# Optimization experiments

Measured on AMD Instinct MI355X. Metric: run time of the kernel, lower is better.

Reference implementation:

```python
import jax, jax.numpy as jnp
import numpy as np


def _moe(x, router_w, bias, shared_up, shared_down, expert_up, expert_down, topk):
    B, T, C = x.shape
    xf = x.reshape(-1, C)                      # (N, C)
    N = xf.shape[0]
    E = router_w.shape[1]
    P = N * topk
    capacity = 2 * P // E

    # --- shared SwiGLU expert (always active); torch Expert order: (y, gate) = chunk ---
    y, g = jnp.split(xf @ shared_up, 2, axis=-1)
    shared = (jax.nn.silu(g) * y) @ shared_down          # (N, C)

    # --- sigmoid top-k gate with (detached) load-balance bias ---
    scores = jax.nn.sigmoid(xf @ router_w)               # (N, E)
    _, topk_idx = jax.lax.top_k(jax.lax.stop_gradient(scores) + bias, topk)  # (N, K)
    w = jnp.take_along_axis(scores, topk_idx, axis=-1)
    w = w / jnp.sum(w, axis=-1, keepdims=True)           # route_scale = 1.0

    # --- token permutation: sort (token, k) pairs by expert id (stable) ---
    pair_e = topk_idx.reshape(-1)                        # (P,)
    pair_t = jnp.repeat(jnp.arange(N), topk)             # (P,) original token ids
    pair_w = w.reshape(-1)
    order = jnp.argsort(pair_e, stable=True)
    se, st, sw = pair_e[order], pair_t[order], pair_w[order]
    counts = jnp.bincount(pair_e, length=E)              # tokens per expert
    offs = jnp.cumsum(counts) - counts                   # start of each expert's slice
    pos = jnp.arange(P) - offs[se]                       # slot within expert group (< capacity)

    # --- grouped-GEMM expert execution via capacity-padded (E, cap, C) buffer ---
    xbuf = jnp.zeros((E, capacity, C), x.dtype).at[se, pos].set(xf[st])
    up = jnp.einsum('epc,ech->eph', xbuf, expert_up)     # (E, cap, 2*He)
    y2, g2 = jnp.split(up, 2, axis=-1)
    h = jax.nn.silu(g2) * y2
    oe = jnp.einsum('eph,ehc->epc', h, expert_down)      # (E, cap, C)

    # --- weighted combine back to original token positions ---
    out_pairs = oe[se, pos] * sw[:, None]                # (P, C)
    out = jnp.zeros_like(xf).at[st].add(out_pairs)
    return (shared + out).reshape(B, T, C)


def setup_inputs() -> dict:
    key = jax.random.key(0)
    ks = jax.random.split(key, 6)
    B, T, C, E, He, Hs, K = 2, 2048, 1024, 64, 512, 1024, 8
    s = 0.02
    return {
        'x': jax.random.normal(ks[0], (B, T, C), jnp.float32),
        'router_w': jax.random.normal(ks[1], (C, E), jnp.float32) * s,
        'bias': jnp.zeros((E,), jnp.float32),
        'shared_up': jax.random.normal(ks[2], (C, 2 * Hs), jnp.float32) * s,
        'shared_down': jax.random.normal(ks[3], (Hs, C), jnp.float32) * s,
        'expert_up': jax.random.normal(ks[4], (E, C, 2 * He), jnp.float32) * s,
        'expert_down': jax.random.normal(ks[5], (E, He, C), jnp.float32) * s,
        'topk': K,
    }


def reference(x, router_w, bias, shared_up, shared_down, expert_up, expert_down, topk):
    return _moe(x, router_w, bias, shared_up, shared_down, expert_up, expert_down, topk)
```

## Files before the change

kernel.cpp:

```cpp
#include <hip/hip_runtime.h>
#include <stdint.h>

#define N_TOK 4096
#define C_DIM 1024
#define E_NUM 64
#define TOPK  8
#define P_PAIR (N_TOK*TOPK)
#define RMAX  40960

typedef __attribute__((ext_vector_type(8))) short bf16x8;
typedef __attribute__((ext_vector_type(4))) float f32x4;

__device__ __forceinline__ uint32_t f2bf(float f){
  uint32_t u = __builtin_bit_cast(uint32_t, f);
  u += 0x7fffu + ((u >> 16) & 1u);
  return u >> 16;
}
__device__ __forceinline__ uint32_t pack2bf(float a, float b){
  uint32_t ua = __builtin_bit_cast(uint32_t, a);
  uint32_t ub = __builtin_bit_cast(uint32_t, b);
  ua += 0x7fffu + ((ua >> 16) & 1u);
  ub += 0x7fffu + ((ub >> 16) & 1u);
  return (ua >> 16) | (ub & 0xffff0000u);
}
__device__ __forceinline__ float bf2f(uint32_t u){
  return __builtin_bit_cast(float, u << 16);
}

__global__ __launch_bounds__(256) void router_scores(
    const float* __restrict__ x, const float* __restrict__ rw, double* __restrict__ scores)
{
  __shared__ float xs[16][C_DIM];
  int t0 = blockIdx.x * 16;
  for (int r = 0; r < 16; ++r) {
    int c = threadIdx.x * 4;
    *(float4*)&xs[r][c] = *(const float4*)&x[(size_t)(t0 + r)*C_DIM + c];
  }
  __syncthreads();
  int e = threadIdx.x & 63;
  int slot = threadIdx.x >> 6;
  double acc0=0, acc1=0, acc2=0, acc3=0;
  for (int c = 0; c < C_DIM; ++c) {
    double w = (double)rw[c*E_NUM + e];
    acc0 += (double)xs[slot    ][c] * w;
    acc1 += (double)xs[slot + 4][c] * w;
    acc2 += (double)xs[slot + 8][c] * w;
    acc3 += (double)xs[slot +12][c] * w;
  }
  scores[(size_t)(t0 + slot     )*E_NUM + e] = 1.0/(1.0 + exp(-acc0));
  scores[(size_t)(t0 + slot +  4)*E_NUM + e] = 1.0/(1.0 + exp(-acc1));
  scores[(size_t)(t0 + slot +  8)*E_NUM + e] = 1.0/(1.0 + exp(-acc2));
  scores[(size_t)(t0 + slot + 12)*E_NUM + e] = 1.0/(1.0 + exp(-acc3));
}

__global__ __launch_bounds__(256) void router_topk(
    const double* __restrict__ scores, const float* __restrict__ bias,
    int* __restrict__ topk_idx, float* __restrict__ topk_w, int* __restrict__ counts)
{
  int t = blockIdx.x * blockDim.x + threadIdx.x;
  if (t >= N_TOK) return;
  const double* s = scores + (size_t)t*E_NUM;
  unsigned long long chosen = 0;
  int idx[TOPK]; double val[TOPK]; double wsum = 0;
  for (int k = 0; k < TOPK; ++k) {
    double best = -1e300; int bi = 0;
    for (int e = 0; e < E_NUM; ++e) {
      if ((chosen >> e) & 1ull) continue;
      double v = s[e] + (double)bias[e];
      if (v > best) { best = v; bi = e; }
    }
    chosen |= 1ull << bi;
    idx[k] = bi;
    val[k] = s[bi];
    wsum += s[bi];
    atomicAdd(&counts[bi], 1);
  }
  for (int k = 0; k < TOPK; ++k) {
    topk_idx[t*TOPK + k] = idx[k];
    topk_w[t*TOPK + k] = (float)(val[k] / wsum);
  }
}

__global__ __launch_bounds__(64) void scan_offsets(const int* __restrict__ counts, int* __restrict__ pad_off)
{
  if (threadIdx.x == 0) {
    int acc = 0;
    for (int e = 0; e < E_NUM; ++e) { pad_off[e] = acc; acc += (counts[e] + 127) & ~127; }
    pad_off[E_NUM] = acc;
  }
}

__global__ __launch_bounds__(256) void build_rows(
    const int* __restrict__ topk_idx, const float* __restrict__ topk_w,
    const int* __restrict__ counts, const int* __restrict__ pad_off,
    int* __restrict__ row_token, float* __restrict__ row_wt, int* __restrict__ row_pair)
{
  int e = blockIdx.x;
  int base = pad_off[e];
  __shared__ int wsum_l[4];
  __shared__ int run_s;
  if (threadIdx.x == 0) run_s = 0;
  int lane = threadIdx.x & 63, wv = threadIdx.x >> 6;
  for (int p0 = 0; p0 < P_PAIR; p0 += 256) {
    int p = p0 + threadIdx.x;
    bool flag = (topk_idx[p] == e);
    unsigned long long mb = __ballot(flag);
    int rank = __popcll(mb & ((1ull << lane) - 1ull));
    if (lane == 0) wsum_l[wv] = __popcll(mb);
    __syncthreads();
    int wbase = 0;
    #pragma unroll
    for (int i = 0; i < 4; ++i) if (i < wv) wbase += wsum_l[i];
    int tot = wsum_l[0] + wsum_l[1] + wsum_l[2] + wsum_l[3];
    int run = run_s;
    if (flag) {
      int row = base + run + wbase + rank;
      row_token[row] = p >> 3;
      row_wt[row]    = topk_w[p];
      row_pair[row]  = p;
    }
    __syncthreads();
    if (threadIdx.x == 0) run_s = run + tot;
  }
  __syncthreads();
  int cnt = counts[e];
  int pc = pad_off[e+1] - base;
  for (int r = cnt + threadIdx.x; r < pc; r += 256) {
    row_token[base + r] = -1;
    row_wt[base + r] = 0.f;
    row_pair[base + r] = -1;
  }
}

template<bool SHARED>
__global__ __launch_bounds__(256) void up_gemm(
    const float* __restrict__ X, const float* __restrict__ Wb,
    const int* __restrict__ row_token, const int* __restrict__ pad_off,
    uint16_t* __restrict__ hout, int ldB, int gOff, int ldh)
{
  __shared__ __align__(16) short As[128*32];
  __shared__ __align__(16) short Bs[128*32];
  __shared__ int tok_lds[128];

  const int tid = threadIdx.x;
  const int e = blockIdx.z;
  int row0;
  if constexpr (SHARED) {
    row0 = blockIdx.y * 128;
  } else {
    int pbase = pad_off[e];
    int pcnt  = pad_off[e+1] - pbase;
    if ((int)blockIdx.y * 128 >= pcnt) return;
    row0 = pbase + blockIdx.y * 128;
  }
  const float* W = Wb + (size_t)e * C_DIM * ldB;
  const int c0 = blockIdx.x * 64;

  if (tid < 128) {
    if constexpr (SHARED) tok_lds[tid] = row0 + tid;
    else                  tok_lds[tid] = row_token[row0 + tid];
  }

  const int lane = tid & 63, wid = tid >> 6;
  const int wm = (wid >> 1) * 64, wn = (wid & 1) * 64;
  const int q = lane >> 4, l15 = lane & 15;

  f32x4 acc[4][4];
  #pragma unroll
  for (int i = 0; i < 4; ++i)
    #pragma unroll
    for (int j = 0; j < 4; ++j) { f32x4 z = {0.f,0.f,0.f,0.f}; acc[i][j] = z; }

  const int lnB = tid & 127;
  const int ucB = ((lnB & 16) ? gOff : 0) + c0 + ((lnB >> 5) << 4) + (lnB & 15);
  const int kgB0 = tid >> 7;
  const int sA = tid & 7, rbA = tid >> 3;

  for (int kt = 0; kt < C_DIM/32; ++kt) {
    const int k0 = kt * 32;
    __syncthreads();
    #pragma unroll
    for (int p = 0; p < 4; ++p) {
      int r = p*32 + rbA;
      int tok = tok_lds[r];
      float4 v = {0.f,0.f,0.f,0.f};
      if (SHARED || tok >= 0) v = *(const float4*)&X[(size_t)tok*C_DIM + k0 + sA*4];
      uint32_t lo = pack2bf(v.x, v.y), hi = pack2bf(v.z, v.w);
      int off = r*32 + ((((sA>>1) ^ (r&3))) << 3) + (sA&1)*4;
      *(uint2*)&As[off] = make_uint2(lo, hi);
    }
    #pragma unroll
    for (int p = 0; p < 4; ++p) {
      int kg = kgB0 + 2*p;
      int kk = k0 + kg*4;
      float v0 = W[(size_t)(kk+0)*ldB + ucB];
      float v1 = W[(size_t)(kk+1)*ldB + ucB];
      float v2 = W[(size_t)(kk+2)*ldB + ucB];
      float v3 = W[(size_t)(kk+3)*ldB + ucB];
      uint32_t lo = pack2bf(v0, v1), hi = pack2bf(v2, v3);
      int off = lnB*32 + ((((kg>>1) ^ (lnB&3))) << 3) + (kg&1)*4;
      *(uint2*)&Bs[off] = make_uint2(lo, hi);
    }
    __syncthreads();
    bf16x8 a[4], b[4];
    #pragma unroll
    for (int mi = 0; mi < 4; ++mi) {
      int r = wm + mi*16 + l15;
      a[mi] = *(const bf16x8*)&As[r*32 + ((q ^ (r&3)) << 3)];
    }
    #pragma unroll
    for (int ni = 0; ni < 4; ++ni) {
      int r = wn + ni*16 + l15;
      b[ni] = *(const bf16x8*)&Bs[r*32 + ((q ^ (r&3)) << 3)];
    }
    #pragma unroll
    for (int mi = 0; mi < 4; ++mi)
      #pragma unroll
      for (int ni = 0; ni < 4; ++ni)
        acc[mi][ni] = __builtin_amdgcn_mfma_f32_16x16x32_bf16(a[mi], b[ni], acc[mi][ni], 0, 0, 0);
  }

  #pragma unroll
  for (int mi = 0; mi < 4; ++mi) {
    int rowb = row0 + wm + mi*16 + q*4;
    #pragma unroll
    for (int jj = 0; jj < 2; ++jj) {
      f32x4 yv = acc[mi][2*jj], gv = acc[mi][2*jj+1];
      int j = (wn >> 5) + jj;
      int hc = c0 + j*16 + l15;
      #pragma unroll
      for (int r = 0; r < 4; ++r) {
        float g = gv[r];
        float sg = 1.f / (1.f + __expf(-g));
        float h = yv[r] * (g * sg);
        hout[(size_t)(rowb + r) * ldh + hc] = (uint16_t)f2bf(h);
      }
    }
  }
}

template<bool SHARED>
__global__ __launch_bounds__(256) void down_gemm(
    const uint16_t* __restrict__ H, const float* __restrict__ Wb,
    const float* __restrict__ row_wt, const int* __restrict__ row_pair,
    const int* __restrict__ pad_off, void* __restrict__ outp,
    int ldh, int Kdim)
{
  __shared__ __align__(16) short As[128*32];
  __shared__ __align__(16) short Bs[128*32];
  __shared__ float wt_lds[128];
  __shared__ int pr_lds[128];

  const int tid = threadIdx.x;
  const int e = blockIdx.z;
  int row0;
  if constexpr (SHARED) {
    row0 = blockIdx.y * 128;
  } else {
    int pbase = pad_off[e];
    int pcnt  = pad_off[e+1] - pbase;
    if ((int)blockIdx.y * 128 >= pcnt) return;
    row0 = pbase + blockIdx.y * 128;
  }
  const float* W = Wb + (size_t)e * Kdim * 1024;
  const int c0 = blockIdx.x * 128;

  if (!SHARED && tid < 128) {
    wt_lds[tid] = row_wt[row0 + tid];
    pr_lds[tid] = row_pair[row0 + tid];
  }

  const int lane = tid & 63, wid = tid >> 6;
  const int wm = (wid >> 1) * 64, wn = (wid & 1) * 64;
  const int q = lane >> 4, l15 = lane & 15;

  f32x4 acc[4][4];
  #pragma unroll
  for (int i = 0; i < 4; ++i)
    #pragma unroll
    for (int j = 0; j < 4; ++j) { f32x4 z = {0.f,0.f,0.f,0.f}; acc[i][j] = z; }

  const int lnB = tid & 127;
  const int kgB0 = tid >> 7;
  const int rbA = tid >> 2, cA = tid & 3;

  const int KT = Kdim >> 5;
  for (int kt = 0; kt < KT; ++kt) {
    const int k0 = kt * 32;
    __syncthreads();
    #pragma unroll
    for (int p = 0; p < 2; ++p) {
      int r = p*64 + rbA;
      uint4 v = *(const uint4*)&H[(size_t)(row0 + r)*ldh + k0 + cA*8];
      int off = r*32 + ((cA ^ (r&3)) << 3);
      *(uint4*)&As[off] = v;
    }
    #pragma unroll
    for (int p = 0; p < 4; ++p) {
      int kg = kgB0 + 2*p;
      int kk = k0 + kg*4;
      float v0 = W[(size_t)(kk+0)*1024 + c0 + lnB];
      float v1 = W[(size_t)(kk+1)*1024 + c0 + lnB];
      float v2 = W[(size_t)(kk+2)*1024 + c0 + lnB];
      float v3 = W[(size_t)(kk+3)*1024 + c0 + lnB];
      uint32_t lo = pack2bf(v0, v1), hi = pack2bf(v2, v3);
      int off = lnB*32 + ((((kg>>1) ^ (lnB&3))) << 3) + (kg&1)*4;
      *(uint2*)&Bs[off] = make_uint2(lo, hi);
    }
    __syncthreads();
    bf16x8 a[4], b[4];
    #pragma unroll
    for (int mi = 0; mi < 4; ++mi) {
      int r = wm + mi*16 + l15;
      a[mi] = *(const bf16x8*)&As[r*32 + ((q ^ (r&3)) << 3)];
    }
    #pragma unroll
    for (int ni = 0; ni < 4; ++ni) {
      int r = wn + ni*16 + l15;
      b[ni] = *(const bf16x8*)&Bs[r*32 + ((q ^ (r&3)) << 3)];
    }
    #pragma unroll
    for (int mi = 0; mi < 4; ++mi)
      #pragma unroll
      for (int ni = 0; ni < 4; ++ni)
        acc[mi][ni] = __builtin_amdgcn_mfma_f32_16x16x32_bf16(a[mi], b[ni], acc[mi][ni], 0, 0, 0);
  }

  if constexpr (SHARED) {
    float* out = (float*)outp;
    #pragma unroll
    for (int mi = 0; mi < 4; ++mi) {
      int rowb = row0 + wm + mi*16 + q*4;
      #pragma unroll
      for (int r = 0; r < 4; ++r)
        #pragma unroll
        for (int ni = 0; ni < 4; ++ni)
          out[(size_t)(rowb + r)*1024 + c0 + wn + ni*16 + l15] = acc[mi][ni][r];
    }
  } else {
    uint16_t* ob = (uint16_t*)outp;
    #pragma unroll
    for (int mi = 0; mi < 4; ++mi) {
      int rloc = wm + mi*16 + q*4;
      #pragma unroll
      for (int r = 0; r < 4; ++r) {
        float wt = wt_lds[rloc + r];
        int pr = pr_lds[rloc + r];
        if (pr >= 0) {
          #pragma unroll
          for (int ni = 0; ni < 4; ++ni)
            ob[(size_t)pr*1024 + c0 + wn + ni*16 + l15] = (uint16_t)f2bf(acc[mi][ni][r] * wt);
        }
      }
    }
  }
}

__global__ __launch_bounds__(256) void combine_kernel(
    const uint16_t* __restrict__ obuf, float* __restrict__ out)
{
  int t = blockIdx.x;
  int c = threadIdx.x * 4;
  float a0=0, a1=0, a2=0, a3=0;
  #pragma unroll
  for (int k = 0; k < TOPK; ++k) {
    uint2 v = *(const uint2*)&obuf[((size_t)t*TOPK + k)*1024 + c];
    a0 += bf2f(v.x & 0xffffu); a1 += bf2f(v.x >> 16);
    a2 += bf2f(v.y & 0xffffu); a3 += bf2f(v.y >> 16);
  }
  float4 o = *(float4*)&out[(size_t)t*1024 + c];
  o.x += a0; o.y += a1; o.z += a2; o.w += a3;
  *(float4*)&out[(size_t)t*1024 + c] = o;
}

extern "C" void kernel_launch(void* const* d_in, const int* in_sizes, int n_in,
                              void* d_out, int out_size, void* d_ws, size_t ws_size,
                              hipStream_t stream)
{
  const float* x           = (const float*)d_in[0];
  const float* router_w    = (const float*)d_in[1];
  const float* bias        = (const float*)d_in[2];
  const float* shared_up   = (const float*)d_in[3];
  const float* shared_down = (const float*)d_in[4];
  const float* expert_up   = (const float*)d_in[5];
  const float* expert_down = (const float*)d_in[6];
  float* out = (float*)d_out;

  char* w = (char*)d_ws;
  auto alloc = [&](size_t bytes) -> void* {
    void* p = (void*)w;
    w += (bytes + 255) & ~(size_t)255;
    return p;
  };
  double*  scores    = (double*)  alloc((size_t)N_TOK*E_NUM*8);
  int*     topk_idx  = (int*)     alloc((size_t)N_TOK*TOPK*4);
  float*   topk_w    = (float*)   alloc((size_t)N_TOK*TOPK*4);
  int*     counts    = (int*)     alloc(E_NUM*4);
  int*     pad_off   = (int*)     alloc((E_NUM+1)*4);
  int*     row_token = (int*)     alloc((size_t)RMAX*4);
  float*   row_wt    = (float*)   alloc((size_t)RMAX*4);
  int*     row_pair  = (int*)     alloc((size_t)RMAX*4);
  uint16_t* hbuf     = (uint16_t*)alloc((size_t)RMAX*512*2);
  uint16_t* hsbuf    = (uint16_t*)alloc((size_t)N_TOK*1024*2);
  uint16_t* obuf     = (uint16_t*)alloc((size_t)P_PAIR*1024*2);

  hipMemsetAsync(counts, 0, E_NUM*4, stream);
  router_scores<<<N_TOK/16, 256, 0, stream>>>(x, router_w, scores);
  router_topk<<<N_TOK/256, 256, 0, stream>>>(scores, bias, topk_idx, topk_w, counts);
  scan_offsets<<<1, 64, 0, stream>>>(counts, pad_off);
  build_rows<<<E_NUM, 256, 0, stream>>>(topk_idx, topk_w, counts, pad_off, row_token, row_wt, row_pair);

  up_gemm<false><<<dim3(8, 8, 64), 256, 0, stream>>>(x, expert_up, row_token, pad_off, hbuf, 1024, 512, 512);
  up_gemm<true><<<dim3(16, 32, 1), 256, 0, stream>>>(x, shared_up, nullptr, nullptr, hsbuf, 2048, 1024, 1024);
  down_gemm<true><<<dim3(8, 32, 1), 256, 0, stream>>>(hsbuf, shared_down, nullptr, nullptr, nullptr, (void*)out, 1024, 1024);
  down_gemm<false><<<dim3(8, 8, 64), 256, 0, stream>>>(hbuf, expert_down, row_wt, row_pair, pad_off, (void*)obuf, 512, 512);
  combine_kernel<<<N_TOK, 256, 0, stream>>>(obuf, out);
}
```

Baseline: 1.299 ms.

## Pre-convert weights to transposed bf16 and stream GEMM tiles via global_load_lds

Adds per-call kernels that convert x to bf16 and transpose-convert all expert and shared weights to bf16 in K-contiguous layout. The GEMMs then fill LDS with direct 16-byte global-to-LDS async copies in MFMA fragment order, replacing the per-element fp32 loads and in-register bf16 packing. The expert grids are also flattened with a remapped block order that interleaves experts. The trade-off is an extra pass that reads all fp32 weights (about 400MB) and writes them back as bf16 on every call, in exchange for cheaper, coalesced GEMM operand loads.

Result: faster. 1.117 ms (-14.0%).

```diff
diff --git a/kernel.cpp b/kernel.cpp
--- a/kernel.cpp
+++ b/kernel.cpp
@@ -10,21 +10,27 @@
 
 typedef __attribute__((ext_vector_type(8))) short bf16x8;
 typedef __attribute__((ext_vector_type(4))) float f32x4;
-
-__device__ __forceinline__ uint32_t f2bf(float f){
-  uint32_t u = __builtin_bit_cast(uint32_t, f);
+typedef uint32_t u32;
+
+__device__ __forceinline__ u32 f2bf(float f){
+  u32 u = __builtin_bit_cast(u32, f);
   u += 0x7fffu + ((u >> 16) & 1u);
   return u >> 16;
 }
-__device__ __forceinline__ uint32_t pack2bf(float a, float b){
-  uint32_t ua = __builtin_bit_cast(uint32_t, a);
-  uint32_t ub = __builtin_bit_cast(uint32_t, b);
+__device__ __forceinline__ u32 pack2bf(float a, float b){
+  u32 ua = __builtin_bit_cast(u32, a);
+  u32 ub = __builtin_bit_cast(u32, b);
   ua += 0x7fffu + ((ua >> 16) & 1u);
   ub += 0x7fffu + ((ub >> 16) & 1u);
   return (ua >> 16) | (ub & 0xffff0000u);
 }
-__device__ __forceinline__ float bf2f(uint32_t u){
+__device__ __forceinline__ float bf2f(u32 u){
   return __builtin_bit_cast(float, u << 16);
+}
+
+__device__ __forceinline__ void async_copy16(const void* g, void* l) {
+  __builtin_amdgcn_global_load_lds((const __attribute__((address_space(1))) u32*)g,
+                                   (__attribute__((address_space(3))) u32*)l, 16, 0, 0);
 }
 
 __global__ __launch_bounds__(256) void router_scores(
@@ -132,38 +138,94 @@
   }
 }
 
+__global__ __launch_bounds__(256) void cvt_x(const float* __restrict__ in, uint16_t* __restrict__ out)
+{
+  int i = blockIdx.x * 256 + threadIdx.x;
+  float4 a = *(const float4*)&in[(size_t)i*8];
+  float4 b = *(const float4*)&in[(size_t)i*8 + 4];
+  uint4 o;
+  o.x = pack2bf(a.x, a.y); o.y = pack2bf(a.z, a.w);
+  o.z = pack2bf(b.x, b.y); o.w = pack2bf(b.z, b.w);
+  *(uint4*)&out[(size_t)i*8] = o;
+}
+
+__global__ __launch_bounds__(256) void transpose_cvt(
+    const float* __restrict__ in, uint16_t* __restrict__ out, int R, int Cc)
+{
+  __shared__ uint16_t tile[64][72];
+  const size_t bo = (size_t)blockIdx.z * R * Cc;
+  int c0 = blockIdx.x * 64;
+  int r0 = blockIdx.y * 64;
+  int tx = threadIdx.x & 15, ty = threadIdx.x >> 4;
+  #pragma unroll
+  for (int i = 0; i < 4; ++i) {
+    int r = ty + i*16;
+    float4 v = *(const float4*)&in[bo + (size_t)(r0 + r)*Cc + c0 + tx*4];
+    *(uint2*)&tile[r][tx*4] = make_uint2(pack2bf(v.x, v.y), pack2bf(v.z, v.w));
+  }
+  __syncthreads();
+  #pragma unroll
+  for (int i = 0; i < 2; ++i) {
+    int u = threadIdx.x + 256*i;
+    int c = u >> 3, rc = u & 7;
+    uint16_t tmp[8];
+    #pragma unroll
+    for (int j = 0; j < 8; ++j) tmp[j] = tile[rc*8 + j][c];
+    *(uint4*)&out[bo + (size_t)(c0 + c)*R + r0 + rc*8] = *(uint4*)tmp;
+  }
+}
+
 template<bool SHARED>
-__global__ __launch_bounds__(256) void up_gemm(
-    const float* __restrict__ X, const float* __restrict__ Wb,
+__global__ __launch_bounds__(256) void up_gemm2(
+    const uint16_t* __restrict__ Xb, const uint16_t* __restrict__ Wt,
     const int* __restrict__ row_token, const int* __restrict__ pad_off,
-    uint16_t* __restrict__ hout, int ldB, int gOff, int ldh)
-{
-  __shared__ __align__(16) short As[128*32];
-  __shared__ __align__(16) short Bs[128*32];
+    uint16_t* __restrict__ hout, int He, int ldh)
+{
+  __shared__ __align__(16) uint16_t As[8*512];
+  __shared__ __align__(16) uint16_t Bs[8*512];
   __shared__ int tok_lds[128];
 
   const int tid = threadIdx.x;
-  const int e = blockIdx.z;
+  int e, xt, yt;
+  if constexpr (SHARED) {
+    e = 0; xt = blockIdx.x; yt = blockIdx.y;
+  } else {
+    int f = blockIdx.x;
+    int s = f >> 3;
+    e = (f & 7) * 8 + (s >> 6);
+    int unit = s & 63;
+    xt = unit & 7; yt = unit >> 3;
+  }
   int row0;
   if constexpr (SHARED) {
-    row0 = blockIdx.y * 128;
+    row0 = yt * 128;
   } else {
-    int pbase = pad_off[e];
-    int pcnt  = pad_off[e+1] - pbase;
-    if ((int)blockIdx.y * 128 >= pcnt) return;
-    row0 = pbase + blockIdx.y * 128;
-  }
-  const float* W = Wb + (size_t)e * C_DIM * ldB;
-  const int c0 = blockIdx.x * 64;
-
-  if (tid < 128) {
-    if constexpr (SHARED) tok_lds[tid] = row0 + tid;
-    else                  tok_lds[tid] = row_token[row0 + tid];
-  }
+    int pbase = pad_off[e], pcnt = pad_off[e+1] - pbase;
+    if (yt * 128 >= pcnt) return;
+    row0 = pbase + yt * 128;
+  }
+  const int c0 = xt * 64;
+  const uint16_t* W = Wt + (size_t)e * (2*He) * 1024;
+
+  if (tid < 128)
+    tok_lds[tid] = SHARED ? (row0 + tid) : row_token[row0 + tid];
+  __syncthreads();
 
   const int lane = tid & 63, wid = tid >> 6;
+  const int l15 = lane & 15, q = lane >> 4;
   const int wm = (wid >> 1) * 64, wn = (wid & 1) * 64;
-  const int q = lane >> 4, l15 = lane & 15;
+
+  const int gp0 = 2*wid, gp1 = 2*wid + 1;
+  int tA0 = tok_lds[gp0*16 + l15]; if (tA0 < 0) tA0 = 0;
+  int tA1 = tok_lds[gp1*16 + l15]; if (tA1 < 0) tA1 = 0;
+  const uint16_t* gA0 = Xb + (size_t)tA0*C_DIM + q*8;
+  const uint16_t* gA1 = Xb + (size_t)tA1*C_DIM + q*8;
+  const int nc0 = ((gp0 & 1) ? He : 0) + c0 + (gp0 >> 1)*16 + l15;
+  const int nc1 = ((gp1 & 1) ? He : 0) + c0 + (gp1 >> 1)*16 + l15;
+  const uint16_t* gB0 = W + (size_t)nc0*C_DIM + q*8;
+  const uint16_t* gB1 = W + (size_t)nc1*C_DIM + q*8;
+  uint16_t* lA0 = &As[gp0*512]; uint16_t* lA1 = &As[gp1*512];
+  uint16_t* lB0 = &Bs[gp0*512]; uint16_t* lB1 = &Bs[gp1*512];
 
   f32x4 acc[4][4];
   #pragma unroll
@@ -171,48 +233,20 @@
     #pragma unroll
     for (int j = 0; j < 4; ++j) { f32x4 z = {0.f,0.f,0.f,0.f}; acc[i][j] = z; }
 
-  const int lnB = tid & 127;
-  const int ucB = ((lnB & 16) ? gOff : 0) + c0 + ((lnB >> 5) << 4) + (lnB & 15);
-  const int kgB0 = tid >> 7;
-  const int sA = tid & 7, rbA = tid >> 3;
-
-  for (int kt = 0; kt < C_DIM/32; ++kt) {
-    const int k0 = kt * 32;
-    __syncthreads();
-    #pragma unroll
-    for (int p = 0; p < 4; ++p) {
-      int r = p*32 + rbA;
-      int tok = tok_lds[r];
-      float4 v = {0.f,0.f,0.f,0.f};
-      if (SHARED || tok >= 0) v = *(const float4*)&X[(size_t)tok*C_DIM + k0 + sA*4];
-      uint32_t lo = pack2bf(v.x, v.y), hi = pack2bf(v.z, v.w);
-      int off = r*32 + ((((sA>>1) ^ (r&3))) << 3) + (sA&1)*4;
-      *(uint2*)&As[off] = make_uint2(lo, hi);
-    }
-    #pragma unroll
-    for (int p = 0; p < 4; ++p) {
-      int kg = kgB0 + 2*p;
-      int kk = k0 + kg*4;
-      float v0 = W[(size_t)(kk+0)*ldB + ucB];
-      float v1 = W[(size_t)(kk+1)*ldB + ucB];
-      float v2 = W[(size_t)(kk+2)*ldB + ucB];
-      float v3 = W[(size_t)(kk+3)*ldB + ucB];
-      uint32_t lo = pack2bf(v0, v1), hi = pack2bf(v2, v3);
-      int off = lnB*32 + ((((kg>>1) ^ (lnB&3))) << 3) + (kg&1)*4;
-      *(uint2*)&Bs[off] = make_uint2(lo, hi);
-    }
+  for (int k0 = 0; k0 < C_DIM; k0 += 32) {
+    __syncthreads();
+    async_copy16(gA0 + k0, lA0);
+    async_copy16(gA1 + k0, lA1);
+    async_copy16(gB0 + k0, lB0);
+    async_copy16(gB1 + k0, lB1);
     __syncthreads();
     bf16x8 a[4], b[4];
     #pragma unroll
-    for (int mi = 0; mi < 4; ++mi) {
-      int r = wm + mi*16 + l15;
-      a[mi] = *(const bf16x8*)&As[r*32 + ((q ^ (r&3)) << 3)];
-    }
-    #pragma unroll
-    for (int ni = 0; ni < 4; ++ni) {
-      int r = wn + ni*16 + l15;
-      b[ni] = *(const bf16x8*)&Bs[r*32 + ((q ^ (r&3)) << 3)];
-    }
+    for (int mi = 0; mi < 4; ++mi)
+      a[mi] = *(const bf16x8*)&As[(wm/16 + mi)*512 + lane*8];
+    #pragma unroll
+    for (int ni = 0; ni < 4; ++ni)
+      b[ni] = *(const bf16x8*)&Bs[(wn/16 + ni)*512 + lane*8];
     #pragma unroll
     for (int mi = 0; mi < 4; ++mi)
       #pragma unroll
@@ -240,39 +274,56 @@
 }
 
 template<bool SHARED>
-__global__ __launch_bounds__(256) void down_gemm(
-    const uint16_t* __restrict__ H, const float* __restrict__ Wb,
+__global__ __launch_bounds__(256) void down_gemm2(
+    const uint16_t* __restrict__ H, const uint16_t* __restrict__ Wt,
     const float* __restrict__ row_wt, const int* __restrict__ row_pair,
     const int* __restrict__ pad_off, void* __restrict__ outp,
     int ldh, int Kdim)
 {
-  __shared__ __align__(16) short As[128*32];
-  __shared__ __align__(16) short Bs[128*32];
+  __shared__ __align__(16) uint16_t As[8*512];
+  __shared__ __align__(16) uint16_t Bs[8*512];
   __shared__ float wt_lds[128];
   __shared__ int pr_lds[128];
 
   const int tid = threadIdx.x;
-  const int e = blockIdx.z;
+  int e, xt, yt;
+  if constexpr (SHARED) {
+    e = 0; xt = blockIdx.x; yt = blockIdx.y;
+  } else {
+    int f = blockIdx.x;
+    int s = f >> 3;
+    e = (f & 7) * 8 + (s >> 6);
+    int unit = s & 63;
+    xt = unit & 7; yt = unit >> 3;
+  }
   int row0;
   if constexpr (SHARED) {
-    row0 = blockIdx.y * 128;
+    row0 = yt * 128;
   } else {
-    int pbase = pad_off[e];
-    int pcnt  = pad_off[e+1] - pbase;
-    if ((int)blockIdx.y * 128 >= pcnt) return;
-    row0 = pbase + blockIdx.y * 128;
-  }
-  const float* W = Wb + (size_t)e * Kdim * 1024;
-  const int c0 = blockIdx.x * 128;
+    int pbase = pad_off[e], pcnt = pad_off[e+1] - pbase;
+    if (yt * 128 >= pcnt) return;
+    row0 = pbase + yt * 128;
+  }
+  const int c0 = xt * 128;
+  const uint16_t* W = Wt + (size_t)e * 1024 * Kdim;
 
   if (!SHARED && tid < 128) {
     wt_lds[tid] = row_wt[row0 + tid];
     pr_lds[tid] = row_pair[row0 + tid];
   }
+  __syncthreads();
 
   const int lane = tid & 63, wid = tid >> 6;
+  const int l15 = lane & 15, q = lane >> 4;
   const int wm = (wid >> 1) * 64, wn = (wid & 1) * 64;
-  const int q = lane >> 4, l15 = lane & 15;
+
+  const int gp0 = 2*wid, gp1 = 2*wid + 1;
+  const uint16_t* gA0 = H + (size_t)(row0 + gp0*16 + l15)*ldh + q*8;
+  const uint16_t* gA1 = H + (size_t)(row0 + gp1*16 + l15)*ldh + q*8;
+  const uint16_t* gB0 = W + (size_t)(c0 + gp0*16 + l15)*Kdim + q*8;
+  const uint16_t* gB1 = W + (size_t)(c0 + gp1*16 + l15)*Kdim + q*8;
+  uint16_t* lA0 = &As[gp0*512]; uint16_t* lA1 = &As[gp1*512];
+  uint16_t* lB0 = &Bs[gp0*512]; uint16_t* lB1 = &Bs[gp1*512];
 
   f32x4 acc[4][4];
   #pragma unroll
@@ -280,45 +331,20 @@
     #pragma unroll
     for (int j = 0; j < 4; ++j) { f32x4 z = {0.f,0.f,0.f,0.f}; acc[i][j] = z; }
 
-  const int lnB = tid & 127;
-  const int kgB0 = tid >> 7;
-  const int rbA = tid >> 2, cA = tid & 3;
-
-  const int KT = Kdim >> 5;
-  for (int kt = 0; kt < KT; ++kt) {
-    const int k0 = kt * 32;
-    __syncthreads();
-    #pragma unroll
-    for (int p = 0; p < 2; ++p) {
-      int r = p*64 + rbA;
-      uint4 v = *(const uint4*)&H[(size_t)(row0 + r)*ldh + k0 + cA*8];
-      int off = r*32 + ((cA ^ (r&3)) << 3);
-      *(uint4*)&As[off] = v;
-    }
-    #pragma unroll
-    for (int p = 0; p < 4; ++p) {
-      int kg = kgB0 + 2*p;
-      int kk = k0 + kg*4;
-      float v0 = W[(size_t)(kk+0)*1024 + c0 + lnB];
-      float v1 = W[(size_t)(kk+1)*1024 + c0 + lnB];
-      float v2 = W[(size_t)(kk+2)*1024 + c0 + lnB];
-      float v3 = W[(size_t)(kk+3)*1024 + c0 + lnB];
-      uint32_t lo = pack2bf(v0, v1), hi = pack2bf(v2, v3);
-      int off = lnB*32 + ((((kg>>1) ^ (lnB&3))) << 3) + (kg&1)*4;
-      *(uint2*)&Bs[off] = make_uint2(lo, hi);
-    }
+  for (int k0 = 0; k0 < Kdim; k0 += 32) {
+    __syncthreads();
+    async_copy16(gA0 + k0, lA0);
+    async_copy16(gA1 + k0, lA1);
+    async_copy16(gB0 + k0, lB0);
+    async_copy16(gB1 + k0, lB1);
     __syncthreads();
     bf16x8 a[4], b[4];
     #pragma unroll
-    for (int mi = 0; mi < 4; ++mi) {
-      int r = wm + mi*16 + l15;
-      a[mi] = *(const bf16x8*)&As[r*32 + ((q ^ (r&3)) << 3)];
-    }
-    #pragma unroll
-    for (int ni = 0; ni < 4; ++ni) {
-      int r = wn + ni*16 + l15;
-      b[ni] = *(const bf16x8*)&Bs[r*32 + ((q ^ (r&3)) << 3)];
-    }
+    for (int mi = 0; mi < 4; ++mi)
+      a[mi] = *(const bf16x8*)&As[(wm/16 + mi)*512 + lane*8];
+    #pragma unroll
+    for (int ni = 0; ni < 4; ++ni)
+      b[ni] = *(const bf16x8*)&Bs[(wn/16 + ni)*512 + lane*8];
     #pragma unroll
     for (int mi = 0; mi < 4; ++mi)
       #pragma unroll
@@ -400,19 +426,31 @@
   int*     row_token = (int*)     alloc((size_t)RMAX*4);
   float*   row_wt    = (float*)   alloc((size_t)RMAX*4);
   int*     row_pair  = (int*)     alloc((size_t)RMAX*4);
+  uint16_t* xbf      = (uint16_t*)alloc((size_t)N_TOK*C_DIM*2);
+  uint16_t* eup_t    = (uint16_t*)alloc((size_t)E_NUM*1024*1024*2);
+  uint16_t* edn_t    = (uint16_t*)alloc((size_t)E_NUM*1024*512*2);
+  uint16_t* sup_t    = (uint16_t*)alloc((size_t)2048*1024*2);
+  uint16_t* sdn_t    = (uint16_t*)alloc((size_t)1024*1024*2);
   uint16_t* hbuf     = (uint16_t*)alloc((size_t)RMAX*512*2);
   uint16_t* hsbuf    = (uint16_t*)alloc((size_t)N_TOK*1024*2);
   uint16_t* obuf     = (uint16_t*)alloc((size_t)P_PAIR*1024*2);
 
   hipMemsetAsync(counts, 0, E_NUM*4, stream);
+
+  cvt_x<<<(N_TOK*C_DIM)/(256*8), 256, 0, stream>>>(x, xbf);
+  transpose_cvt<<<dim3(16, 16, 64), 256, 0, stream>>>(expert_up,   eup_t, 1024, 1024);
+  transpose_cvt<<<dim3(16,  8, 64), 256, 0, stream>>>(expert_down, edn_t,  512, 1024);
+  transpose_cvt<<<dim3(32, 16,  1), 256, 0, stream>>>(shared_up,   sup_t, 1024, 2048);
+  transpose_cvt<<<dim3(16, 16,  1), 256, 0, stream>>>(shared_down, sdn_t, 1024, 1024);
+
   router_scores<<<N_TOK/16, 256, 0, stream>>>(x, router_w, scores);
   router_topk<<<N_TOK/256, 256, 0, stream>>>(scores, bias, topk_idx, topk_w, counts);
   scan_offsets<<<1, 64, 0, stream>>>(counts, pad_off);
   build_rows<<<E_NUM, 256, 0, stream>>>(topk_idx, topk_w, counts, pad_off, row_token, row_wt, row_pair);
 
-  up_gemm<false><<<dim3(8, 8, 64), 256, 0, stream>>>(x, expert_up, row_token, pad_off, hbuf, 1024, 512, 512);
-  up_gemm<true><<<dim3(16, 32, 1), 256, 0, stream>>>(x, shared_up, nullptr, nullptr, hsbuf, 2048, 1024, 1024);
-  down_gemm<true><<<dim3(8, 32, 1), 256, 0, stream>>>(hsbuf, shared_down, nullptr, nullptr, nullptr, (void*)out, 1024, 1024);
-  down_gemm<false><<<dim3(8, 8, 64), 256, 0, stream>>>(hbuf, expert_down, row_wt, row_pair, pad_off, (void*)obuf, 512, 512);
+  up_gemm2<false><<<4096, 256, 0, stream>>>(xbf, eup_t, row_token, pad_off, hbuf, 512, 512);
+  up_gemm2<true><<<dim3(16, 32), 256, 0, stream>>>(xbf, sup_t, nullptr, nullptr, hsbuf, 1024, 1024);
+  down_gemm2<true><<<dim3(8, 32), 256, 0, stream>>>(hsbuf, sdn_t, nullptr, nullptr, nullptr, (void*)out, 1024, 1024);
+  down_gemm2<false><<<4096, 256, 0, stream>>>(hbuf, edn_t, row_wt, row_pair, pad_off, (void*)obuf, 512, 512);
   combine_kernel<<<N_TOK, 256, 0, stream>>>(obuf, out);
 }
```
